# Kernel tuning notes

Measured on AMD Instinct MI355X. Metric: run time of the kernel, lower is better.

## Reference

```python
import jax, jax.numpy as jnp
import numpy as np

N_NODES = 100000
IN_CH, HID_CH, OUT_CH = 128, 256, 128
N_EDGES = 1600000


def setup_inputs() -> dict:
    key = jax.random.key(0)
    ks = jax.random.split(key, 12)
    x = jax.random.normal(ks[0], (N_NODES, IN_CH), dtype=jnp.float32)
    edge_index = jax.random.randint(ks[1], (2, N_EDGES), 0, N_NODES, dtype=jnp.int32)
    s1 = 1.0 / np.sqrt(IN_CH)
    s2 = 1.0 / np.sqrt(HID_CH)
    return {
        "x": x,
        "edge_index": edge_index,
        "eps1": jnp.zeros((), jnp.float32),
        "W1a": jax.random.uniform(ks[2], (IN_CH, HID_CH), jnp.float32, -s1, s1),
        "b1a": jax.random.uniform(ks[3], (HID_CH,), jnp.float32, -s1, s1),
        "W1b": jax.random.uniform(ks[4], (HID_CH, HID_CH), jnp.float32, -s2, s2),
        "b1b": jax.random.uniform(ks[5], (HID_CH,), jnp.float32, -s2, s2),
        "eps2": jnp.zeros((), jnp.float32),
        "W2a": jax.random.uniform(ks[6], (HID_CH, HID_CH), jnp.float32, -s2, s2),
        "b2a": jax.random.uniform(ks[7], (HID_CH,), jnp.float32, -s2, s2),
        "W2b": jax.random.uniform(ks[8], (HID_CH, OUT_CH), jnp.float32, -s2, s2),
        "b2b": jax.random.uniform(ks[9], (OUT_CH,), jnp.float32, -s2, s2),
    }


def _gin_conv(x, src, dst, eps, Wa, ba, Wb, bb):
    # sum-aggregate source features into destinations: [N, d]
    agg = jax.ops.segment_sum(x[src], dst, num_segments=N_NODES)
    h = (1.0 + eps) * x + agg
    h = jax.nn.relu(h @ Wa + ba)
    return h @ Wb + bb


def reference(x, edge_index, eps1, W1a, b1a, W1b, b1b, eps2, W2a, b2a, W2b, b2b):
    src, dst = edge_index[0], edge_index[1]
    h = _gin_conv(x, src, dst, eps1, W1a, b1a, W1b, b1b)
    h = jax.nn.relu(h)
    out = _gin_conv(h, src, dst, eps2, W2a, b2a, W2b, b2b)
    return out
```

## Files before the change

### kernel.cpp

```cpp
#include <hip/hip_runtime.h>

#define N_NODES 100000
#define N_EDGES 1600000
#define NB 782
#define BSTRIDE 32

typedef __attribute__((ext_vector_type(8))) short short8;
typedef __attribute__((ext_vector_type(4))) float float4e;

#define GLDS16(g, l)                                                   \
  __builtin_amdgcn_global_load_lds(                                    \
      (const __attribute__((address_space(1))) unsigned int*)(g),      \
      (__attribute__((address_space(3))) unsigned int*)(l), 16, 0, 0)

__device__ __forceinline__ unsigned short f2bf(float f) {
  unsigned u = __float_as_uint(f);
  u += 0x7FFFu + ((u >> 16) & 1u);
  return (unsigned short)(u >> 16);
}
__device__ __forceinline__ float bf2f(unsigned short h) {
  return __uint_as_float(((unsigned)h) << 16);
}

__global__ __launch_bounds__(256) void bucketHist_k(const int* __restrict__ dst,
                                                    int* __restrict__ bucketCnt,
                                                    int nE) {
  __shared__ int h[1024];
  for (int j = threadIdx.x; j < 1024; j += 256) h[j] = 0;
  __syncthreads();
  const int stride = gridDim.x * 256;
  for (int i = blockIdx.x * 256 + threadIdx.x; i < nE; i += stride)
    atomicAdd(&h[dst[i] >> 7], 1);
  __syncthreads();
  for (int j = threadIdx.x; j < NB; j += 256) {
    int v = h[j];
    if (v) atomicAdd(&bucketCnt[j * BSTRIDE], v);
  }
}

__global__ __launch_bounds__(1024) void scanB_k(const int* __restrict__ bucketCnt,
                                                int* __restrict__ bucketStart,
                                                int* __restrict__ bucketCursor) {
  __shared__ int sm[1024];
  const int tid = threadIdx.x;
  int v = (tid < NB) ? bucketCnt[tid * BSTRIDE] : 0;
  sm[tid] = v;
  __syncthreads();
  for (int off = 1; off < 1024; off <<= 1) {
    int t = (tid >= off) ? sm[tid - off] : 0;
    __syncthreads();
    sm[tid] += t;
    __syncthreads();
  }
  if (tid < NB) {
    int excl = sm[tid] - v;
    bucketStart[tid] = excl;
    bucketCursor[tid * BSTRIDE] = excl;
  }
  if (tid == NB - 1) bucketStart[NB] = sm[tid];
}

__global__ __launch_bounds__(256) void bucketScatter_k(
    const int* __restrict__ src, const int* __restrict__ dst,
    int* __restrict__ bucketCursor, unsigned int* __restrict__ packed, int nE) {
  int i = blockIdx.x * 256 + threadIdx.x;
  if (i < nE) {
    int d = dst[i];
    int p = atomicAdd(&bucketCursor[(d >> 7) * BSTRIDE], 1);
    packed[p] = ((unsigned)src[i] << 7) | (unsigned)(d & 127);
  }
}

__global__ __launch_bounds__(256) void fillB_k(
    const int* __restrict__ bucketStart, const unsigned int* __restrict__ packed,
    int* __restrict__ rowEnd, int* __restrict__ sortedSrc, int nNodes) {
  __shared__ int cnt[128];
  __shared__ int cur[128];
  const int b = blockIdx.x;
  const int tid = threadIdx.x;
  const int s0 = bucketStart[b];
  const int ne = bucketStart[b + 1] - s0;
  if (tid < 128) cnt[tid] = 0;
  __syncthreads();
  for (int i = tid; i < ne; i += 256)
    atomicAdd(&cnt[packed[s0 + i] & 127u], 1);
  __syncthreads();
  int v = (tid < 128) ? cnt[tid] : 0;
  for (int off = 1; off < 128; off <<= 1) {
    int t = (tid < 128 && tid >= off) ? cnt[tid - off] : 0;
    __syncthreads();
    if (tid < 128) cnt[tid] += t;
    __syncthreads();
  }
  if (tid < 128) {
    cur[tid] = s0 + cnt[tid] - v;
    int node = b * 128 + tid;
    if (node < nNodes) rowEnd[node] = s0 + cnt[tid];
  }
  __syncthreads();
  for (int i = tid; i < ne; i += 256) {
    unsigned p = packed[s0 + i];
    int idx = atomicAdd(&cur[p & 127u], 1);
    sortedSrc[idx] = (int)(p >> 7);
  }
}

__global__ __launch_bounds__(256) void wprep_k(
    const float* __restrict__ W, unsigned short* __restrict__ th,
    unsigned short* __restrict__ tl, int K, int N) {
  int i = blockIdx.x * blockDim.x + threadIdx.x;
  if (i < K * N) {
    int k = i / N, n = i % N;
    float v = W[i];
    unsigned short h = f2bf(v);
    unsigned short l = f2bf(v - bf2f(h));
    th[(long)n * K + k] = h;
    tl[(long)n * K + k] = l;
  }
}

__global__ __launch_bounds__(256) void xprep_k(const float* __restrict__ x,
                                               unsigned short* __restrict__ xh,
                                               int n) {
  int i = blockIdx.x * blockDim.x + threadIdx.x;
  if (i < n) xh[i] = f2bf(x[i]);
}

template <int C, bool XF32>
__global__ __launch_bounds__(256) void agg_g16_k(
    const unsigned short* __restrict__ feat_h, const float* __restrict__ xf,
    const unsigned short* __restrict__ xh, const unsigned short* __restrict__ xl,
    const float* __restrict__ epsp, const int* __restrict__ rowEnd,
    const int* __restrict__ sortedSrc, unsigned short* __restrict__ oh,
    unsigned short* __restrict__ ol, int M) {
  constexpr int V = C / 64;
  const int lane = threadIdx.x & 63;
  const int w = (int)((blockIdx.x * blockDim.x + threadIdx.x) >> 6);
  if (w >= M) return;
  const int start = w ? rowEnd[w - 1] : 0;
  const int end = rowEnd[w];
  const int c0 = lane * V;

  float acc[V] = {};
  int e = start;
  for (; e + 8 <= end; e += 8) {
    int si[8];
#pragma unroll
    for (int q = 0; q < 8; ++q) si[q] = sortedSrc[e + q];
    if constexpr (V == 4) {
      ushort4 t[8];
#pragma unroll
      for (int q = 0; q < 8; ++q)
        t[q] = *(const ushort4*)(feat_h + (long)si[q] * C + c0);
#pragma unroll
      for (int q = 0; q < 8; ++q) {
        acc[0] += bf2f(t[q].x);
        acc[1] += bf2f(t[q].y);
        acc[2] += bf2f(t[q].z);
        acc[3] += bf2f(t[q].w);
      }
    } else {
      ushort2 t[8];
#pragma unroll
      for (int q = 0; q < 8; ++q)
        t[q] = *(const ushort2*)(feat_h + (long)si[q] * C + c0);
#pragma unroll
      for (int q = 0; q < 8; ++q) {
        acc[0] += bf2f(t[q].x);
        acc[1] += bf2f(t[q].y);
      }
    }
  }
  for (; e + 4 <= end; e += 4) {
    int s0 = sortedSrc[e + 0];
    int s1 = sortedSrc[e + 1];
    int s2 = sortedSrc[e + 2];
    int s3 = sortedSrc[e + 3];
    if constexpr (V == 4) {
      ushort4 a = *(const ushort4*)(feat_h + (long)s0 * C + c0);
      ushort4 b = *(const ushort4*)(feat_h + (long)s1 * C + c0);
      ushort4 c = *(const ushort4*)(feat_h + (long)s2 * C + c0);
      ushort4 d = *(const ushort4*)(feat_h + (long)s3 * C + c0);
      acc[0] += bf2f(a.x) + bf2f(b.x) + bf2f(c.x) + bf2f(d.x);
      acc[1] += bf2f(a.y) + bf2f(b.y) + bf2f(c.y) + bf2f(d.y);
      acc[2] += bf2f(a.z) + bf2f(b.z) + bf2f(c.z) + bf2f(d.z);
      acc[3] += bf2f(a.w) + bf2f(b.w) + bf2f(c.w) + bf2f(d.w);
    } else {
      ushort2 a = *(const ushort2*)(feat_h + (long)s0 * C + c0);
      ushort2 b = *(const ushort2*)(feat_h + (long)s1 * C + c0);
      ushort2 c = *(const ushort2*)(feat_h + (long)s2 * C + c0);
      ushort2 d = *(const ushort2*)(feat_h + (long)s3 * C + c0);
      acc[0] += bf2f(a.x) + bf2f(b.x) + bf2f(c.x) + bf2f(d.x);
      acc[1] += bf2f(a.y) + bf2f(b.y) + bf2f(c.y) + bf2f(d.y);
    }
  }
  for (; e < end; ++e) {
    const unsigned short* r = feat_h + (long)sortedSrc[e] * C + c0;
    if constexpr (V == 4) {
      ushort4 a = *(const ushort4*)r;
      acc[0] += bf2f(a.x); acc[1] += bf2f(a.y);
      acc[2] += bf2f(a.z); acc[3] += bf2f(a.w);
    } else {
      ushort2 a = *(const ushort2*)r;
      acc[0] += bf2f(a.x); acc[1] += bf2f(a.y);
    }
  }

  const float s = 1.0f + epsp[0];
  float xv[V];
  if constexpr (XF32) {
#pragma unroll
    for (int v = 0; v < V; ++v) xv[v] = xf[(long)w * C + c0 + v];
  } else {
#pragma unroll
    for (int v = 0; v < V; ++v)
      xv[v] = bf2f(xh[(long)w * C + c0 + v]) + bf2f(xl[(long)w * C + c0 + v]);
  }

  unsigned short hv[V], lv[V];
#pragma unroll
  for (int v = 0; v < V; ++v) {
    float res = fmaf(s, xv[v], acc[v]);
    hv[v] = f2bf(res);
    lv[v] = f2bf(res - bf2f(hv[v]));
  }
  if constexpr (V == 4) {
    *(ushort4*)&oh[(long)w * C + c0] = make_ushort4(hv[0], hv[1], hv[2], hv[3]);
    *(ushort4*)&ol[(long)w * C + c0] = make_ushort4(lv[0], lv[1], lv[2], lv[3]);
  } else {
    *(ushort2*)&oh[(long)w * C + c0] = make_ushort2(hv[0], hv[1]);
    *(ushort2*)&ol[(long)w * C + c0] = make_ushort2(lv[0], lv[1]);
  }
}

template <int NFRAG, bool RELU, bool HILO>
__global__ __launch_bounds__(256, 3) void gemm_wide_k(
    const unsigned short* __restrict__ Ah, const unsigned short* __restrict__ Al,
    const unsigned short* __restrict__ Bth, const unsigned short* __restrict__ Btl,
    const float* __restrict__ bias, float* __restrict__ outf,
    unsigned short* __restrict__ oh, unsigned short* __restrict__ ol,
    int M, int K) {
  constexpr int N = NFRAG * 16;
  __shared__ unsigned short Ahs[64 * 32];
  __shared__ unsigned short Als[64 * 32];
  __shared__ unsigned short Bhs[N * 32];
  __shared__ unsigned short Bls[N * 32];

  const int tid = threadIdx.x;
  const int lane = tid & 63;
  const int wave = tid >> 6;
  const int l15 = lane & 15;
  const int quad = lane >> 4;
  const int m0 = blockIdx.x * 64;

  float4e acc[NFRAG];
#pragma unroll
  for (int j = 0; j < NFRAG; ++j) acc[j] = 0.0f;

  const int a_row = tid >> 2;
  const int a_col = (tid & 3) * 8;
  const bool a_ok = (m0 + a_row) < M;

  for (int k0 = 0; k0 < K; k0 += 32) {
    {
      long ga = (long)(m0 + a_row) * K + k0 + a_col;
      if (a_ok) {
        GLDS16(Ah + ga, &Ahs[tid * 8]);
        GLDS16(Al + ga, &Als[tid * 8]);
      }
    }
#pragma unroll
    for (int u = 0; u < NFRAG / 4; ++u) {
      int c = u * 256 + tid;
      long gb = (long)(c >> 2) * K + k0 + (c & 3) * 8;
      GLDS16(Bth + gb, &Bhs[c * 8]);
      GLDS16(Btl + gb, &Bls[c * 8]);
    }
    __syncthreads();

    short8 a_h = *(const short8*)&Ahs[(wave * 16 + l15) * 32 + quad * 8];
    short8 a_l = *(const short8*)&Als[(wave * 16 + l15) * 32 + quad * 8];

#pragma unroll
    for (int j = 0; j < NFRAG; ++j) {
      short8 b_h = *(const short8*)&Bhs[(j * 16 + l15) * 32 + quad * 8];
      short8 b_l = *(const short8*)&Bls[(j * 16 + l15) * 32 + quad * 8];
      acc[j] = __builtin_amdgcn_mfma_f32_16x16x32_bf16(a_h, b_h, acc[j], 0, 0, 0);
      acc[j] = __builtin_amdgcn_mfma_f32_16x16x32_bf16(a_h, b_l, acc[j], 0, 0, 0);
      acc[j] = __builtin_amdgcn_mfma_f32_16x16x32_bf16(a_l, b_h, acc[j], 0, 0, 0);
    }
    __syncthreads();
  }

#pragma unroll
  for (int j = 0; j < NFRAG; ++j) {
    int col = j * 16 + l15;
    float bj = bias[col];
    int rbase = m0 + wave * 16 + quad * 4;
#pragma unroll
    for (int r = 0; r < 4; ++r) {
      int row = rbase + r;
      if (row < M) {
        float v = acc[j][r] + bj;
        if constexpr (RELU) v = fmaxf(v, 0.0f);
        if constexpr (HILO) {
          unsigned short h = f2bf(v);
          oh[(long)row * N + col] = h;
          ol[(long)row * N + col] = f2bf(v - bf2f(h));
        } else {
          outf[(long)row * N + col] = v;
        }
      }
    }
  }
}

extern "C" void kernel_launch(void* const* d_in, const int* in_sizes, int n_in,
                              void* d_out, int out_size, void* d_ws, size_t ws_size,
                              hipStream_t stream) {
  const float* x    = (const float*)d_in[0];
  const int*   ei   = (const int*)d_in[1];
  const float* eps1 = (const float*)d_in[2];
  const float* W1a  = (const float*)d_in[3];
  const float* b1a  = (const float*)d_in[4];
  const float* W1b  = (const float*)d_in[5];
  const float* b1b  = (const float*)d_in[6];
  const float* eps2 = (const float*)d_in[7];
  const float* W2a  = (const float*)d_in[8];
  const float* b2a  = (const float*)d_in[9];
  const float* W2b  = (const float*)d_in[10];
  const float* b2b  = (const float*)d_in[11];
  float* out = (float*)d_out;

  const int* srcp = ei;
  const int* dstp = ei + N_EDGES;

  char* ws = (char*)d_ws;
  const size_t SZ = (size_t)N_NODES * 256 * sizeof(float);
  char* P1 = ws;
  char* P2 = ws + SZ;

  unsigned short* C1h = (unsigned short*)P1;
  unsigned short* C1l = C1h + (size_t)N_NODES * 128;
  unsigned short* xh  = C1l + (size_t)N_NODES * 128;
  unsigned short* T1h = (unsigned short*)P2;
  unsigned short* T1l = T1h + (size_t)N_NODES * 256;
  unsigned short* Hh = (unsigned short*)P1;
  unsigned short* Hl = Hh + (size_t)N_NODES * 256;
  unsigned short* C2h = (unsigned short*)P2;
  unsigned short* C2l = C2h + (size_t)N_NODES * 256;
  unsigned short* T2h = (unsigned short*)P1;
  unsigned short* T2l = T2h + (size_t)N_NODES * 256;
  unsigned short* W2bh = (unsigned short*)P2;
  unsigned short* W2bl = W2bh + 128 * 256;

  char* ob = (char*)d_out;
  int* rowEnd    = (int*)(ob + 400 * 1024);
  int* sortedSrc = (int*)(ob + 800 * 1024);
  size_t wofs = 7340032;
  unsigned short* W1ah = (unsigned short*)(ob + wofs);
  unsigned short* W1al = W1ah + 256 * 128;
  unsigned short* W1bh = (unsigned short*)(ob + wofs + 2 * 65536);
  unsigned short* W1bl = W1bh + 256 * 256;
  unsigned short* W2ah = (unsigned short*)(ob + wofs + 2 * 65536 + 2 * 131072);
  unsigned short* W2al = W2ah + 256 * 256;
  unsigned int* packed = (unsigned int*)(ob + 16 * 1024 * 1024);
  int* bucketCnt    = (int*)(ob + 24 * 1024 * 1024);
  int* bucketCursor = (int*)(ob + 26 * 1024 * 1024);
  int* bucketStart  = (int*)(ob + 28 * 1024 * 1024);

  dim3 blk(256);
  dim3 gEdges((N_EDGES + 255) / 256);
  dim3 gAgg((N_NODES + 3) / 4);
  dim3 gGemm((N_NODES + 63) / 64);
  dim3 gW1((128 * 256 + 255) / 256);
  dim3 gW2((256 * 256 + 255) / 256);
  dim3 gXp((N_NODES * 128 + 255) / 256);

  hipMemsetAsync(bucketCnt, 0, NB * BSTRIDE * sizeof(int), stream);
  bucketHist_k<<<dim3(512), blk, 0, stream>>>(dstp, bucketCnt, N_EDGES);
  scanB_k<<<1, dim3(1024), 0, stream>>>(bucketCnt, bucketStart, bucketCursor);
  bucketScatter_k<<<gEdges, blk, 0, stream>>>(srcp, dstp, bucketCursor, packed,
                                              N_EDGES);
  fillB_k<<<dim3(NB), blk, 0, stream>>>(bucketStart, packed, rowEnd, sortedSrc,
                                        N_NODES);
  xprep_k<<<gXp, blk, 0, stream>>>(x, xh, N_NODES * 128);
  wprep_k<<<gW1, blk, 0, stream>>>(W1a, W1ah, W1al, 128, 256);
  wprep_k<<<gW2, blk, 0, stream>>>(W1b, W1bh, W1bl, 256, 256);
  wprep_k<<<gW2, blk, 0, stream>>>(W2a, W2ah, W2al, 256, 256);

  agg_g16_k<128, true><<<gAgg, blk, 0, stream>>>(
      xh, x, nullptr, nullptr, eps1, rowEnd, sortedSrc, C1h, C1l, N_NODES);
  gemm_wide_k<16, true, true><<<gGemm, blk, 0, stream>>>(
      C1h, C1l, W1ah, W1al, b1a, nullptr, T1h, T1l, N_NODES, 128);
  gemm_wide_k<16, true, true><<<gGemm, blk, 0, stream>>>(
      T1h, T1l, W1bh, W1bl, b1b, nullptr, Hh, Hl, N_NODES, 256);

  agg_g16_k<256, false><<<gAgg, blk, 0, stream>>>(
      Hh, nullptr, Hh, Hl, eps2, rowEnd, sortedSrc, C2h, C2l, N_NODES);
  gemm_wide_k<16, true, true><<<gGemm, blk, 0, stream>>>(
      C2h, C2l, W2ah, W2al, b2a, nullptr, T2h, T2l, N_NODES, 256);
  wprep_k<<<gW1, blk, 0, stream>>>(W2b, W2bh, W2bl, 256, 128);
  gemm_wide_k<8, false, false><<<gGemm, blk, 0, stream>>>(
      T2h, T2l, W2bh, W2bl, b2b, out, nullptr, nullptr, N_NODES, 256);
}
```

Baseline: 753.5 us.

## Double-buffer GEMM LDS tiles and split layer-2 aggregation into column halves

The GEMM kernel now double-buffers its LDS tiles, so the next K-slice's global-to-LDS loads are issued before computing on the current slice. Because this doubles LDS use, the occupancy hint drops to 2 blocks per CU for the wide GEMMs. The aggregation kernel becomes a generic 2-column-per-lane version with a row stride and column offset. The 256-wide layer-2 gather now runs as two passes over 128-column halves, shrinking each pass's gather working set to improve cache hit rates. In exchange, the edge index list is read twice and there is one extra kernel launch.

```diff
diff --git a/kernel.cpp b/kernel.cpp
--- a/kernel.cpp
+++ b/kernel.cpp
@@ -126,20 +126,20 @@
   if (i < n) xh[i] = f2bf(x[i]);
 }
 
-template <int C, bool XF32>
-__global__ __launch_bounds__(256) void agg_g16_k(
+template <bool XF32>
+__global__ __launch_bounds__(256) void agg_s_k(
     const unsigned short* __restrict__ feat_h, const float* __restrict__ xf,
     const unsigned short* __restrict__ xh, const unsigned short* __restrict__ xl,
     const float* __restrict__ epsp, const int* __restrict__ rowEnd,
     const int* __restrict__ sortedSrc, unsigned short* __restrict__ oh,
-    unsigned short* __restrict__ ol, int M) {
-  constexpr int V = C / 64;
+    unsigned short* __restrict__ ol, int M, int S, int off) {
+  constexpr int V = 2;
   const int lane = threadIdx.x & 63;
   const int w = (int)((blockIdx.x * blockDim.x + threadIdx.x) >> 6);
   if (w >= M) return;
   const int start = w ? rowEnd[w - 1] : 0;
   const int end = rowEnd[w];
-  const int c0 = lane * V;
+  const int c0 = lane * V + off;
 
   float acc[V] = {};
   int e = start;
@@ -147,28 +147,14 @@
     int si[8];
 #pragma unroll
     for (int q = 0; q < 8; ++q) si[q] = sortedSrc[e + q];
-    if constexpr (V == 4) {
-      ushort4 t[8];
-#pragma unroll
-      for (int q = 0; q < 8; ++q)
-        t[q] = *(const ushort4*)(feat_h + (long)si[q] * C + c0);
-#pragma unroll
-      for (int q = 0; q < 8; ++q) {
-        acc[0] += bf2f(t[q].x);
-        acc[1] += bf2f(t[q].y);
-        acc[2] += bf2f(t[q].z);
-        acc[3] += bf2f(t[q].w);
-      }
-    } else {
-      ushort2 t[8];
-#pragma unroll
-      for (int q = 0; q < 8; ++q)
-        t[q] = *(const ushort2*)(feat_h + (long)si[q] * C + c0);
-#pragma unroll
-      for (int q = 0; q < 8; ++q) {
-        acc[0] += bf2f(t[q].x);
-        acc[1] += bf2f(t[q].y);
-      }
+    ushort2 t[8];
+#pragma unroll
+    for (int q = 0; q < 8; ++q)
+      t[q] = *(const ushort2*)(feat_h + (long)si[q] * S + c0);
+#pragma unroll
+    for (int q = 0; q < 8; ++q) {
+      acc[0] += bf2f(t[q].x);
+      acc[1] += bf2f(t[q].y);
     }
   }
   for (; e + 4 <= end; e += 4) {
@@ -176,45 +162,28 @@
     int s1 = sortedSrc[e + 1];
     int s2 = sortedSrc[e + 2];
     int s3 = sortedSrc[e + 3];
-    if constexpr (V == 4) {
-      ushort4 a = *(const ushort4*)(feat_h + (long)s0 * C + c0);
-      ushort4 b = *(const ushort4*)(feat_h + (long)s1 * C + c0);
-      ushort4 c = *(const ushort4*)(feat_h + (long)s2 * C + c0);
-      ushort4 d = *(const ushort4*)(feat_h + (long)s3 * C + c0);
-      acc[0] += bf2f(a.x) + bf2f(b.x) + bf2f(c.x) + bf2f(d.x);
-      acc[1] += bf2f(a.y) + bf2f(b.y) + bf2f(c.y) + bf2f(d.y);
-      acc[2] += bf2f(a.z) + bf2f(b.z) + bf2f(c.z) + bf2f(d.z);
-      acc[3] += bf2f(a.w) + bf2f(b.w) + bf2f(c.w) + bf2f(d.w);
-    } else {
-      ushort2 a = *(const ushort2*)(feat_h + (long)s0 * C + c0);
-      ushort2 b = *(const ushort2*)(feat_h + (long)s1 * C + c0);
-      ushort2 c = *(const ushort2*)(feat_h + (long)s2 * C + c0);
-      ushort2 d = *(const ushort2*)(feat_h + (long)s3 * C + c0);
-      acc[0] += bf2f(a.x) + bf2f(b.x) + bf2f(c.x) + bf2f(d.x);
-      acc[1] += bf2f(a.y) + bf2f(b.y) + bf2f(c.y) + bf2f(d.y);
-    }
+    ushort2 a = *(const ushort2*)(feat_h + (long)s0 * S + c0);
+    ushort2 b = *(const ushort2*)(feat_h + (long)s1 * S + c0);
+    ushort2 c = *(const ushort2*)(feat_h + (long)s2 * S + c0);
+    ushort2 d = *(const ushort2*)(feat_h + (long)s3 * S + c0);
+    acc[0] += bf2f(a.x) + bf2f(b.x) + bf2f(c.x) + bf2f(d.x);
+    acc[1] += bf2f(a.y) + bf2f(b.y) + bf2f(c.y) + bf2f(d.y);
   }
   for (; e < end; ++e) {
-    const unsigned short* r = feat_h + (long)sortedSrc[e] * C + c0;
-    if constexpr (V == 4) {
-      ushort4 a = *(const ushort4*)r;
-      acc[0] += bf2f(a.x); acc[1] += bf2f(a.y);
-      acc[2] += bf2f(a.z); acc[3] += bf2f(a.w);
-    } else {
-      ushort2 a = *(const ushort2*)r;
-      acc[0] += bf2f(a.x); acc[1] += bf2f(a.y);
-    }
+    ushort2 a = *(const ushort2*)(feat_h + (long)sortedSrc[e] * S + c0);
+    acc[0] += bf2f(a.x);
+    acc[1] += bf2f(a.y);
   }
 
   const float s = 1.0f + epsp[0];
   float xv[V];
   if constexpr (XF32) {
 #pragma unroll
-    for (int v = 0; v < V; ++v) xv[v] = xf[(long)w * C + c0 + v];
+    for (int v = 0; v < V; ++v) xv[v] = xf[(long)w * S + c0 + v];
   } else {
 #pragma unroll
     for (int v = 0; v < V; ++v)
-      xv[v] = bf2f(xh[(long)w * C + c0 + v]) + bf2f(xl[(long)w * C + c0 + v]);
+      xv[v] = bf2f(xh[(long)w * S + c0 + v]) + bf2f(xl[(long)w * S + c0 + v]);
   }
 
   unsigned short hv[V], lv[V];
@@ -224,27 +193,22 @@
     hv[v] = f2bf(res);
     lv[v] = f2bf(res - bf2f(hv[v]));
   }
-  if constexpr (V == 4) {
-    *(ushort4*)&oh[(long)w * C + c0] = make_ushort4(hv[0], hv[1], hv[2], hv[3]);
-    *(ushort4*)&ol[(long)w * C + c0] = make_ushort4(lv[0], lv[1], lv[2], lv[3]);
-  } else {
-    *(ushort2*)&oh[(long)w * C + c0] = make_ushort2(hv[0], hv[1]);
-    *(ushort2*)&ol[(long)w * C + c0] = make_ushort2(lv[0], lv[1]);
-  }
-}
-
-template <int NFRAG, bool RELU, bool HILO>
-__global__ __launch_bounds__(256, 3) void gemm_wide_k(
+  *(ushort2*)&oh[(long)w * S + c0] = make_ushort2(hv[0], hv[1]);
+  *(ushort2*)&ol[(long)w * S + c0] = make_ushort2(lv[0], lv[1]);
+}
+
+template <int NFRAG, bool RELU, bool HILO, int MINW>
+__global__ __launch_bounds__(256, MINW) void gemm_wide_k(
     const unsigned short* __restrict__ Ah, const unsigned short* __restrict__ Al,
     const unsigned short* __restrict__ Bth, const unsigned short* __restrict__ Btl,
     const float* __restrict__ bias, float* __restrict__ outf,
     unsigned short* __restrict__ oh, unsigned short* __restrict__ ol,
     int M, int K) {
   constexpr int N = NFRAG * 16;
-  __shared__ unsigned short Ahs[64 * 32];
-  __shared__ unsigned short Als[64 * 32];
-  __shared__ unsigned short Bhs[N * 32];
-  __shared__ unsigned short Bls[N * 32];
+  __shared__ unsigned short Ahs[2][64 * 32];
+  __shared__ unsigned short Als[2][64 * 32];
+  __shared__ unsigned short Bhs[2][N * 32];
+  __shared__ unsigned short Bls[2][N * 32];
 
   const int tid = threadIdx.x;
   const int lane = tid & 63;
@@ -261,30 +225,36 @@
   const int a_col = (tid & 3) * 8;
   const bool a_ok = (m0 + a_row) < M;
 
-  for (int k0 = 0; k0 < K; k0 += 32) {
-    {
-      long ga = (long)(m0 + a_row) * K + k0 + a_col;
-      if (a_ok) {
-        GLDS16(Ah + ga, &Ahs[tid * 8]);
-        GLDS16(Al + ga, &Als[tid * 8]);
-      }
+  auto stage = [&](int buf, int k0) {
+    long ga = (long)(m0 + a_row) * K + k0 + a_col;
+    if (a_ok) {
+      GLDS16(Ah + ga, &Ahs[buf][tid * 8]);
+      GLDS16(Al + ga, &Als[buf][tid * 8]);
     }
 #pragma unroll
     for (int u = 0; u < NFRAG / 4; ++u) {
       int c = u * 256 + tid;
       long gb = (long)(c >> 2) * K + k0 + (c & 3) * 8;
-      GLDS16(Bth + gb, &Bhs[c * 8]);
-      GLDS16(Btl + gb, &Bls[c * 8]);
-    }
-    __syncthreads();
-
-    short8 a_h = *(const short8*)&Ahs[(wave * 16 + l15) * 32 + quad * 8];
-    short8 a_l = *(const short8*)&Als[(wave * 16 + l15) * 32 + quad * 8];
+      GLDS16(Bth + gb, &Bhs[buf][c * 8]);
+      GLDS16(Btl + gb, &Bls[buf][c * 8]);
+    }
+  };
+
+  const int nt = K >> 5;
+  stage(0, 0);
+  __syncthreads();
+
+  for (int t = 0; t < nt; ++t) {
+    const int cur = t & 1;
+    if (t + 1 < nt) stage(cur ^ 1, (t + 1) * 32);
+
+    short8 a_h = *(const short8*)&Ahs[cur][(wave * 16 + l15) * 32 + quad * 8];
+    short8 a_l = *(const short8*)&Als[cur][(wave * 16 + l15) * 32 + quad * 8];
 
 #pragma unroll
     for (int j = 0; j < NFRAG; ++j) {
-      short8 b_h = *(const short8*)&Bhs[(j * 16 + l15) * 32 + quad * 8];
-      short8 b_l = *(const short8*)&Bls[(j * 16 + l15) * 32 + quad * 8];
+      short8 b_h = *(const short8*)&Bhs[cur][(j * 16 + l15) * 32 + quad * 8];
+      short8 b_l = *(const short8*)&Bls[cur][(j * 16 + l15) * 32 + quad * 8];
       acc[j] = __builtin_amdgcn_mfma_f32_16x16x32_bf16(a_h, b_h, acc[j], 0, 0, 0);
       acc[j] = __builtin_amdgcn_mfma_f32_16x16x32_bf16(a_h, b_l, acc[j], 0, 0, 0);
       acc[j] = __builtin_amdgcn_mfma_f32_16x16x32_bf16(a_l, b_h, acc[j], 0, 0, 0);
@@ -389,18 +359,20 @@
   wprep_k<<<gW2, blk, 0, stream>>>(W1b, W1bh, W1bl, 256, 256);
   wprep_k<<<gW2, blk, 0, stream>>>(W2a, W2ah, W2al, 256, 256);
 
-  agg_g16_k<128, true><<<gAgg, blk, 0, stream>>>(
-      xh, x, nullptr, nullptr, eps1, rowEnd, sortedSrc, C1h, C1l, N_NODES);
-  gemm_wide_k<16, true, true><<<gGemm, blk, 0, stream>>>(
+  agg_s_k<true><<<gAgg, blk, 0, stream>>>(
+      xh, x, nullptr, nullptr, eps1, rowEnd, sortedSrc, C1h, C1l, N_NODES, 128, 0);
+  gemm_wide_k<16, true, true, 2><<<gGemm, blk, 0, stream>>>(
       C1h, C1l, W1ah, W1al, b1a, nullptr, T1h, T1l, N_NODES, 128);
-  gemm_wide_k<16, true, true><<<gGemm, blk, 0, stream>>>(
+  gemm_wide_k<16, true, true, 2><<<gGemm, blk, 0, stream>>>(
       T1h, T1l, W1bh, W1bl, b1b, nullptr, Hh, Hl, N_NODES, 256);
 
-  agg_g16_k<256, false><<<gAgg, blk, 0, stream>>>(
-      Hh, nullptr, Hh, Hl, eps2, rowEnd, sortedSrc, C2h, C2l, N_NODES);
-  gemm_wide_k<16, true, true><<<gGemm, blk, 0, stream>>>(
+  agg_s_k<false><<<gAgg, blk, 0, stream>>>(
+      Hh, nullptr, Hh, Hl, eps2, rowEnd, sortedSrc, C2h, C2l, N_NODES, 256, 0);
+  agg_s_k<false><<<gAgg, blk, 0, stream>>>(
+      Hh, nullptr, Hh, Hl, eps2, rowEnd, sortedSrc, C2h, C2l, N_NODES, 256, 128);
+  gemm_wide_k<16, true, true, 2><<<gGemm, blk, 0, stream>>>(
       C2h, C2l, W2ah, W2al, b2a, nullptr, T2h, T2l, N_NODES, 256);
   wprep_k<<<gW1, blk, 0, stream>>>(W2b, W2bh, W2bl, 256, 128);
-  gemm_wide_k<8, false, false><<<gGemm, blk, 0, stream>>>(
+  gemm_wide_k<8, false, false, 3><<<gGemm, blk, 0, stream>>>(
       T2h, T2l, W2bh, W2bl, b2b, out, nullptr, nullptr, N_NODES, 256);
 }
```

New measurement: 826.6 us. +9.7%, slower.
